# Kernel optimization log

Measured on AMD Instinct MI355X. Metric: run time of the kernel, lower is better.

The kernel has to match this reference:

```python
import jax, jax.numpy as jnp
import numpy as np

BLOCK = 16  # NVFP4 block size (per-block FP8 scale over 16 FP4 values)
FP4_GRID = jnp.array([0.0, 0.5, 1.0, 1.5, 2.0, 3.0, 4.0, 6.0], dtype=jnp.float32)
FP4_MIDS = jnp.array([0.25, 0.75, 1.25, 1.75, 2.5, 3.5, 5.0], dtype=jnp.float32)


def _quantize_fp4(v):
    # round-to-nearest onto the signed E2M1 grid {0,.5,1,1.5,2,3,4,6}
    a = jnp.clip(jnp.abs(v), 0.0, 6.0)
    idx = jnp.searchsorted(FP4_MIDS, a)
    return jnp.sign(v) * FP4_GRID[idx]


def _block_quantize(x):
    # returns (fp4 values, per-16-block scales) such that x ~= q * scale_blocked
    M, K = x.shape
    B = K // BLOCK
    xb = x.reshape(M, B, BLOCK)
    s = jnp.max(jnp.abs(xb), axis=-1) / 6.0 + 1e-8  # [M, B]
    q = _quantize_fp4(xb / s[:, :, None]).reshape(M, K)
    return q, s


def setup_inputs() -> dict:
    key = jax.random.key(0)
    k1, k2, k3 = jax.random.split(key, 3)
    M, K, N = 8192, 4096, 4096
    bsz, q_len = 4, 2048

    x_raw = jax.random.normal(k1, (M, K), dtype=jnp.float32)
    w_raw = jax.random.normal(k2, (N, K), dtype=jnp.float32) * 0.02

    # global weight scale as in NVFP4_reorder_quantize_w: max(w)/(448*6)
    scale_w_global = jnp.max(w_raw) / (448.0 * 6.0)
    qw, scale_w = _block_quantize(w_raw / scale_w_global)

    # activation global scale (produced upstream by the activation quantizer)
    scale_x_global = jnp.max(x_raw) / (448.0 * 6.0)
    qx, scale_x = _block_quantize(x_raw / scale_x_global)

    bias = jax.random.normal(k3, (N,), dtype=jnp.float32) * 0.01

    return {
        "qx": qx,                      # [M, K] FP4-grid values
        "scale_x": scale_x,            # [M, K//16] block scales
        "scale": scale_x_global,       # scalar global activation scale
        "qw": qw,                      # [N, K] FP4-grid values
        "scale_w": scale_w,            # [N, K//16] block scales
        "scale_w_global": scale_w_global,
        "bias": bias,                  # [N]
        "bsz": bsz,
        "q_len": q_len,
    }


def reference(qx, scale_x, scale, qw, scale_w, scale_w_global, bias, bsz, q_len):
    # Dequant-scaled GEMM: y = (qx .* sx)(qw .* sw)^T * (scale * scale_w_global) + bias
    M, K = qx.shape
    N = qw.shape[0]
    B = K // BLOCK
    xd = (qx.reshape(M, B, BLOCK) * scale_x[:, :, None]).reshape(M, K)
    wd = (qw.reshape(N, B, BLOCK) * scale_w[:, :, None]).reshape(N, K)
    y = jnp.einsum("mk,nk->mn", xd, wd) * (scale * scale_w_global)
    y = y + bias
    return y.reshape(bsz, q_len, -1)
```

## Files before the change

### kernel.cpp

```cpp
#include <hip/hip_runtime.h>
#include <cstdint>

#define K_DIM 4096
#define ROWB 13
#define NT   (K_DIM / 64)

typedef __bf16 bf16x8 __attribute__((ext_vector_type(8)));
typedef float f32x4 __attribute__((ext_vector_type(4)));

__device__ inline unsigned short f2bf(float f) {
    union { float f; unsigned int u; } v; v.f = f;
    unsigned int u = v.u;
    return (unsigned short)((u + 0x7FFFu + ((u >> 16) & 1u)) >> 16);
}

__device__ __forceinline__ void gload16(const void* g, void* l) {
    __builtin_amdgcn_global_load_lds(
        (const __attribute__((address_space(1))) unsigned int*)g,
        (__attribute__((address_space(3))) unsigned int*)l,
        16, 0, 0);
}

__global__ __launch_bounds__(256) void dequant2_kernel(
        const float* __restrict__ qx, const float* __restrict__ sx,
        unsigned short* __restrict__ xd, long t8x,
        const float* __restrict__ qw, const float* __restrict__ sw,
        unsigned short* __restrict__ wd, long t8w) {
    long i = (long)blockIdx.x * blockDim.x + threadIdx.x;
    if (i >= t8x + t8w) return;
    const float* q; const float* s; unsigned short* o;
    if (i < t8x) { q = qx; s = sx; o = xd; }
    else         { q = qw; s = sw; o = wd; i -= t8x; }
    long e = i * 8;
    float sc = s[e >> 4];
    float4 v0 = *(const float4*)(q + e);
    float4 v1 = *(const float4*)(q + e + 4);
    union { unsigned short h[8]; uint4 u; } ov;
    ov.h[0] = f2bf(v0.x * sc); ov.h[1] = f2bf(v0.y * sc);
    ov.h[2] = f2bf(v0.z * sc); ov.h[3] = f2bf(v0.w * sc);
    ov.h[4] = f2bf(v1.x * sc); ov.h[5] = f2bf(v1.y * sc);
    ov.h[6] = f2bf(v1.z * sc); ov.h[7] = f2bf(v1.w * sc);
    *(uint4*)(o + e) = ov.u;
}


__global__ __launch_bounds__(512, 2) void gemm256_kernel(
        const unsigned short* __restrict__ A,
        const unsigned short* __restrict__ B,
        const float* __restrict__ sg1, const float* __restrict__ sg2,
        const float* __restrict__ bias,
        float* __restrict__ out, int M, int N) {
    __shared__ __align__(16) char lds[131072];

    const int tid  = threadIdx.x;
    const int lane = tid & 63;
    const int wid  = tid >> 6;
    const int wm   = wid >> 2;
    const int wn   = wid & 3;
    const int l15  = lane & 15;
    const int cb4  = lane >> 4;
    const int rx   = l15 & 7;
    const int xk0  = (cb4 ^ rx) << 4;
    const int xk1  = ((4 + cb4) ^ rx) << 4;

    const int nbn = N >> 8;
    const int nwg = (M >> 8) * nbn;
    const int cpx = nwg >> 3;
    const int bid = blockIdx.x;
    const int swz = (bid & 7) * cpx + (bid >> 3);
    const int tile_m = (swz / nbn) << 8;
    const int tile_n = (swz % nbn) << 8;

    const int scb = ((lane & 7) ^ ((lane >> 3) & 7)) << 4;
    const char* gA1 = (const char*)A +
        ((size_t)(tile_m + wm * 128 + wn * 16 + (lane >> 3)) << ROWB) + scb;
    const char* gA2 = gA1 + ((size_t)64 << ROWB);
    const char* gBs = (const char*)B +
        ((size_t)(tile_n + wn * 64 + wm * 32 + (lane >> 3)) << ROWB) + scb;
    const int dA1 = (wm * 128 + wn * 16) * 128;
    const int dA2 = dA1 + 8192;
    const int dB  = 32768 + (wn * 64 + wm * 32) * 128;

    const int aB = (wm * 128 + l15) * 128;
    const int bB = 32768 + (wn * 64 + l15) * 128;

    f32x4 acc[8][4];
#pragma unroll
    for (int mb = 0; mb < 8; ++mb)
#pragma unroll
        for (int nb = 0; nb < 4; ++nb) acc[mb][nb] = (f32x4){0.f, 0.f, 0.f, 0.f};

    gload16(gA1, lds + dA1);
    gload16(gA1 + ((size_t)8 << ROWB), lds + dA1 + 1024);
    gload16(gBs, lds + dB);
    gload16(gBs + ((size_t)8 << ROWB), lds + dB + 1024);
    gload16(gBs + ((size_t)16 << ROWB), lds + dB + 2048);
    gload16(gBs + ((size_t)24 << ROWB), lds + dB + 3072);
    gload16(gA2, lds + dA2);
    gload16(gA2 + ((size_t)8 << ROWB), lds + dA2 + 1024);
    asm volatile("s_waitcnt vmcnt(0)" ::: "memory");
    __builtin_amdgcn_s_barrier();

#define TILE_BODY(T, CB, SB) do {                                            \
    const int ts_ = ((T) + 1 < NT) ? (T) + 1 : NT - 1;                       \
    const size_t tso = (size_t)ts_ * 128;                                    \
    bf16x8 af[8], af2[8], bf[4], bf2[4];                                     \
      \
    _Pragma("unroll")                                                        \
    for (int mb = 0; mb < 4; ++mb) {                                         \
        af[mb * 2 + 0] = *(const bf16x8*)(lds + (CB) + aB + mb * 2048 + xk0);\
        af[mb * 2 + 1] = *(const bf16x8*)(lds + (CB) + aB + mb * 2048 + xk1);\
    }                                                                        \
    _Pragma("unroll")                                                        \
    for (int nb = 0; nb < 2; ++nb) {                                         \
        bf[nb * 2 + 0] = *(const bf16x8*)(lds + (CB) + bB + nb * 2048 + xk0);\
        bf[nb * 2 + 1] = *(const bf16x8*)(lds + (CB) + bB + nb * 2048 + xk1);\
    }                                                                        \
    gload16(gA1 + tso, lds + (SB) + dA1);                                    \
    gload16(gA1 + tso + ((size_t)8 << ROWB), lds + (SB) + dA1 + 1024);       \
    __builtin_amdgcn_s_barrier();                                            \
    asm volatile("s_waitcnt lgkmcnt(0)" ::: "memory");                       \
    __builtin_amdgcn_s_setprio(1);                                           \
    _Pragma("unroll")                                                        \
    for (int mb = 0; mb < 4; ++mb)                                           \
        _Pragma("unroll")                                                    \
        for (int nb = 0; nb < 2; ++nb)                                       \
            _Pragma("unroll")                                                \
            for (int ks = 0; ks < 2; ++ks)                                   \
                acc[mb][nb] = __builtin_amdgcn_mfma_f32_16x16x32_bf16(       \
                    af[mb * 2 + ks], bf[nb * 2 + ks], acc[mb][nb], 0, 0, 0); \
    __builtin_amdgcn_s_setprio(0);                                           \
    __builtin_amdgcn_s_barrier();                                            \
        \
    _Pragma("unroll")                                                        \
    for (int nb = 0; nb < 2; ++nb) {                                         \
        bf2[nb * 2 + 0] =                                                    \
            *(const bf16x8*)(lds + (CB) + bB + 4096 + nb * 2048 + xk0);      \
        bf2[nb * 2 + 1] =                                                    \
            *(const bf16x8*)(lds + (CB) + bB + 4096 + nb * 2048 + xk1);      \
    }                                                                        \
    gload16(gBs + tso, lds + (SB) + dB);                                     \
    gload16(gBs + tso + ((size_t)8 << ROWB), lds + (SB) + dB + 1024);        \
    __builtin_amdgcn_s_barrier();                                            \
    asm volatile("s_waitcnt lgkmcnt(0)" ::: "memory");                       \
    __builtin_amdgcn_s_setprio(1);                                           \
    _Pragma("unroll")                                                        \
    for (int mb = 0; mb < 4; ++mb)                                           \
        _Pragma("unroll")                                                    \
        for (int nb = 0; nb < 2; ++nb)                                       \
            _Pragma("unroll")                                                \
            for (int ks = 0; ks < 2; ++ks)                                   \
                acc[mb][2 + nb] = __builtin_amdgcn_mfma_f32_16x16x32_bf16(   \
                    af[mb * 2 + ks], bf2[nb * 2 + ks], acc[mb][2 + nb],      \
                    0, 0, 0);                                                \
    __builtin_amdgcn_s_setprio(0);                                           \
    asm volatile("s_waitcnt vmcnt(4)" ::: "memory");                         \
    __builtin_amdgcn_s_barrier();                                            \
        \
    _Pragma("unroll")                                                        \
    for (int mb = 0; mb < 4; ++mb) {                                         \
        af2[mb * 2 + 0] =                                                    \
            *(const bf16x8*)(lds + (CB) + aB + 8192 + mb * 2048 + xk0);      \
        af2[mb * 2 + 1] =                                                    \
            *(const bf16x8*)(lds + (CB) + aB + 8192 + mb * 2048 + xk1);      \
    }                                                                        \
    gload16(gBs + tso + ((size_t)16 << ROWB), lds + (SB) + dB + 2048);       \
    gload16(gBs + tso + ((size_t)24 << ROWB), lds + (SB) + dB + 3072);       \
    __builtin_amdgcn_s_barrier();                                            \
    asm volatile("s_waitcnt lgkmcnt(0)" ::: "memory");                       \
    __builtin_amdgcn_s_setprio(1);                                           \
    _Pragma("unroll")                                                        \
    for (int mb = 0; mb < 4; ++mb)                                           \
        _Pragma("unroll")                                                    \
        for (int nb = 0; nb < 2; ++nb)                                       \
            _Pragma("unroll")                                                \
            for (int ks = 0; ks < 2; ++ks)                                   \
                acc[4 + mb][2 + nb] = __builtin_amdgcn_mfma_f32_16x16x32_bf16(\
                    af2[mb * 2 + ks], bf2[nb * 2 + ks], acc[4 + mb][2 + nb], \
                    0, 0, 0);                                                \
    __builtin_amdgcn_s_setprio(0);                                           \
    __builtin_amdgcn_s_barrier();                                            \
      \
    gload16(gA2 + tso, lds + (SB) + dA2);                                    \
    gload16(gA2 + tso + ((size_t)8 << ROWB), lds + (SB) + dA2 + 1024);       \
    __builtin_amdgcn_s_setprio(1);                                           \
    _Pragma("unroll")                                                        \
    for (int mb = 0; mb < 4; ++mb)                                           \
        _Pragma("unroll")                                                    \
        for (int nb = 0; nb < 2; ++nb)                                       \
            _Pragma("unroll")                                                \
            for (int ks = 0; ks < 2; ++ks)                                   \
                acc[4 + mb][nb] = __builtin_amdgcn_mfma_f32_16x16x32_bf16(   \
                    af2[mb * 2 + ks], bf[nb * 2 + ks], acc[4 + mb][nb],      \
                    0, 0, 0);                                                \
    __builtin_amdgcn_s_setprio(0);                                           \
    asm volatile("s_waitcnt vmcnt(2)" ::: "memory");                         \
    __builtin_amdgcn_s_barrier();                                            \
} while (0)

    for (int t = 0; t < NT; t += 2) {
        TILE_BODY(t,     0,     65536);
        TILE_BODY(t + 1, 65536, 0);
    }
#undef TILE_BODY

    const float gs = sg1[0] * sg2[0];
    const int row0 = tile_m + wm * 128 + (cb4 << 2);
    const int col0 = tile_n + wn * 64 + l15;
    float bv[4];
#pragma unroll
    for (int nb = 0; nb < 4; ++nb) bv[nb] = bias[col0 + nb * 16];
#pragma unroll
    for (int mb = 0; mb < 8; ++mb)
#pragma unroll
        for (int nb = 0; nb < 4; ++nb) {
            const int col = col0 + nb * 16;
#pragma unroll
            for (int j = 0; j < 4; ++j)
                out[(size_t)(row0 + mb * 16 + j) * N + col] =
                    acc[mb][nb][j] * gs + bv[nb];
        }
}

__global__ __launch_bounds__(256) void gemm_fused_kernel(
        const float* __restrict__ qx, const float* __restrict__ sx,
        const float* __restrict__ qw, const float* __restrict__ sw,
        const float* __restrict__ sg1, const float* __restrict__ sg2,
        const float* __restrict__ bias,
        float* __restrict__ out, int M, int N) {
    __shared__ __align__(16) unsigned short As[128 * 32];
    __shared__ __align__(16) unsigned short Bs[128 * 32];
    const int tid  = threadIdx.x;
    const int lane = tid & 63;
    const int wid  = tid >> 6;
    const int tile_n = blockIdx.x * 128;
    const int tile_m = blockIdx.y * 128;
    const int wm = wid >> 1, wn = wid & 1;
    f32x4 acc[16];
#pragma unroll
    for (int i = 0; i < 16; ++i) acc[i] = (f32x4){0.f, 0.f, 0.f, 0.f};
    const int l15 = lane & 15;
    const int lk  = (lane >> 4) * 8;
    for (int kt = 0; kt < K_DIM / 32; ++kt) {
#pragma unroll
        for (int cc = 0; cc < 2; ++cc) {
            const int c   = tid + cc * 256;
            const int row = c >> 2;
            const int col = (c & 3) * 8;
            const int gk  = kt * 32 + col;
            {
                const float* qp = qx + (long)(tile_m + row) * K_DIM + gk;
                float s = sx[(long)(tile_m + row) * (K_DIM / 16) + (gk >> 4)];
                float4 a0 = *(const float4*)qp;
                float4 a1 = *(const float4*)(qp + 4);
                union { unsigned short h[8]; uint4 u; } o;
                o.h[0] = f2bf(a0.x * s); o.h[1] = f2bf(a0.y * s);
                o.h[2] = f2bf(a0.z * s); o.h[3] = f2bf(a0.w * s);
                o.h[4] = f2bf(a1.x * s); o.h[5] = f2bf(a1.y * s);
                o.h[6] = f2bf(a1.z * s); o.h[7] = f2bf(a1.w * s);
                *(uint4*)&As[row * 32 + col] = o.u;
            }
            {
                const float* qp = qw + (long)(tile_n + row) * K_DIM + gk;
                float s = sw[(long)(tile_n + row) * (K_DIM / 16) + (gk >> 4)];
                float4 a0 = *(const float4*)qp;
                float4 a1 = *(const float4*)(qp + 4);
                union { unsigned short h[8]; uint4 u; } o;
                o.h[0] = f2bf(a0.x * s); o.h[1] = f2bf(a0.y * s);
                o.h[2] = f2bf(a0.z * s); o.h[3] = f2bf(a0.w * s);
                o.h[4] = f2bf(a1.x * s); o.h[5] = f2bf(a1.y * s);
                o.h[6] = f2bf(a1.z * s); o.h[7] = f2bf(a1.w * s);
                *(uint4*)&Bs[row * 32 + col] = o.u;
            }
        }
        __syncthreads();
        const unsigned short* pa = As + (wm * 64 + l15) * 32 + lk;
        const unsigned short* pb = Bs + (wn * 64 + l15) * 32 + lk;
        bf16x8 a[4], b[4];
#pragma unroll
        for (int i = 0; i < 4; ++i) {
            a[i] = *(const bf16x8*)(pa + i * 16 * 32);
            b[i] = *(const bf16x8*)(pb + i * 16 * 32);
        }
#pragma unroll
        for (int mi = 0; mi < 4; ++mi)
#pragma unroll
            for (int ni = 0; ni < 4; ++ni)
                acc[mi * 4 + ni] = __builtin_amdgcn_mfma_f32_16x16x32_bf16(
                    a[mi], b[ni], acc[mi * 4 + ni], 0, 0, 0);
        __syncthreads();
    }
    const float gs = sg1[0] * sg2[0];
    const int row0 = tile_m + wm * 64 + (lane >> 4) * 4;
    const int col0 = tile_n + wn * 64 + l15;
#pragma unroll
    for (int mi = 0; mi < 4; ++mi)
#pragma unroll
        for (int ni = 0; ni < 4; ++ni) {
            const int col = col0 + ni * 16;
            const float bv = bias[col];
#pragma unroll
            for (int j = 0; j < 4; ++j)
                out[(long)(row0 + mi * 16 + j) * N + col] =
                    acc[mi * 4 + ni][j] * gs + bv;
        }
}

extern "C" void kernel_launch(void* const* d_in, const int* in_sizes, int n_in,
                              void* d_out, int out_size, void* d_ws, size_t ws_size,
                              hipStream_t stream) {
    const float* qx   = (const float*)d_in[0];
    const float* sx   = (const float*)d_in[1];
    const float* sc   = (const float*)d_in[2];
    const float* qw   = (const float*)d_in[3];
    const float* sw   = (const float*)d_in[4];
    const float* swg  = (const float*)d_in[5];
    const float* bias = (const float*)d_in[6];
    float* out = (float*)d_out;

    const int M = in_sizes[0] / K_DIM;
    const int N = in_sizes[3] / K_DIM;

    const size_t needA = (size_t)M * K_DIM * sizeof(unsigned short);
    const size_t needB = (size_t)N * K_DIM * sizeof(unsigned short);

    if (ws_size >= needA + needB) {
        unsigned short* xd = (unsigned short*)d_ws;
        unsigned short* wd = (unsigned short*)((char*)d_ws + needA);
        long t8x = (long)M * K_DIM / 8;
        long t8w = (long)N * K_DIM / 8;
        long tot = t8x + t8w;
        dequant2_kernel<<<(int)((tot + 255) / 256), 256, 0, stream>>>(
            qx, sx, xd, t8x, qw, sw, wd, t8w);
        const int nwg = (M / 256) * (N / 256);
        gemm256_kernel<<<nwg, 512, 0, stream>>>(xd, wd, sc, swg, bias, out, M, N);
    } else {
        dim3 grid(N / 128, M / 128);
        gemm_fused_kernel<<<grid, 256, 0, stream>>>(
            qx, sx, qw, sw, sc, swg, bias, out, M, N);
    }
}
```

Measured before the change: 272.1 us.

## Switch GEMM inner loop from 16x16x32 to 32x32x16 bf16 MFMA tiles

Replaces the 16x16x32 bf16 MFMA micro-tiles with 32x32x16 MFMAs. The LDS fragment read addressing, the XOR swizzle offsets, the accumulator layout (f32x16) and the epilogue store mapping change to match. The larger MFMA shape reuses each loaded fragment across more output elements, which cuts LDS reads and MFMA issue count per flop. In exchange, bank-conflict behaviour changes under the new swizzle, and the epilogue writes follow a different row/column pattern.

```diff
diff --git a/kernel.cpp b/kernel.cpp
--- a/kernel.cpp
+++ b/kernel.cpp
@@ -6,7 +6,8 @@
 #define NT   (K_DIM / 64)
 
 typedef __bf16 bf16x8 __attribute__((ext_vector_type(8)));
-typedef float f32x4 __attribute__((ext_vector_type(4)));
+typedef float f32x4  __attribute__((ext_vector_type(4)));
+typedef float f32x16 __attribute__((ext_vector_type(16)));
 
 __device__ inline unsigned short f2bf(float f) {
     union { float f; unsigned int u; } v; v.f = f;
@@ -57,11 +58,13 @@
     const int wid  = tid >> 6;
     const int wm   = wid >> 2;
     const int wn   = wid & 3;
-    const int l15  = lane & 15;
-    const int cb4  = lane >> 4;
-    const int rx   = l15 & 7;
-    const int xk0  = (cb4 ^ rx) << 4;
-    const int xk1  = ((4 + cb4) ^ rx) << 4;
+    const int l31  = lane & 31;
+    const int lhi  = lane >> 5;
+    const int rl7  = lane & 7;
+    const int xs0 = ((0 + lhi) ^ rl7) << 4;
+    const int xs1 = ((2 + lhi) ^ rl7) << 4;
+    const int xs2 = ((4 + lhi) ^ rl7) << 4;
+    const int xs3 = ((6 + lhi) ^ rl7) << 4;
 
     const int nbn = N >> 8;
     const int nwg = (M >> 8) * nbn;
@@ -81,14 +84,16 @@
     const int dA2 = dA1 + 8192;
     const int dB  = 32768 + (wn * 64 + wm * 32) * 128;
 
-    const int aB = (wm * 128 + l15) * 128;
-    const int bB = 32768 + (wn * 64 + l15) * 128;
-
-    f32x4 acc[8][4];
-#pragma unroll
-    for (int mb = 0; mb < 8; ++mb)
-#pragma unroll
-        for (int nb = 0; nb < 4; ++nb) acc[mb][nb] = (f32x4){0.f, 0.f, 0.f, 0.f};
+    const int aB = (wm * 128 + l31) * 128;
+    const int bB = 32768 + (wn * 64 + l31) * 128;
+
+    f32x16 acc[4][2];
+#pragma unroll
+    for (int mb = 0; mb < 4; ++mb)
+#pragma unroll
+        for (int nb = 0; nb < 2; ++nb)
+#pragma unroll
+            for (int j = 0; j < 16; ++j) acc[mb][nb][j] = 0.f;
 
     gload16(gA1, lds + dA1);
     gload16(gA1 + ((size_t)8 << ROWB), lds + dA1 + 1024);
@@ -101,68 +106,62 @@
     asm volatile("s_waitcnt vmcnt(0)" ::: "memory");
     __builtin_amdgcn_s_barrier();
 
+#define RD(P) *(const bf16x8*)(P)
 #define TILE_BODY(T, CB, SB) do {                                            \
     const int ts_ = ((T) + 1 < NT) ? (T) + 1 : NT - 1;                       \
     const size_t tso = (size_t)ts_ * 128;                                    \
-    bf16x8 af[8], af2[8], bf[4], bf2[4];                                     \
-      \
-    _Pragma("unroll")                                                        \
-    for (int mb = 0; mb < 4; ++mb) {                                         \
-        af[mb * 2 + 0] = *(const bf16x8*)(lds + (CB) + aB + mb * 2048 + xk0);\
-        af[mb * 2 + 1] = *(const bf16x8*)(lds + (CB) + aB + mb * 2048 + xk1);\
+    bf16x8 af[2][4], af2[2][4], bf[4], bf2[4];                               \
+        \
+    _Pragma("unroll")                                                        \
+    for (int mb = 0; mb < 2; ++mb) {                                         \
+        af[mb][0] = RD(lds + (CB) + aB + mb * 4096 + xs0);                   \
+        af[mb][1] = RD(lds + (CB) + aB + mb * 4096 + xs1);                   \
+        af[mb][2] = RD(lds + (CB) + aB + mb * 4096 + xs2);                   \
+        af[mb][3] = RD(lds + (CB) + aB + mb * 4096 + xs3);                   \
     }                                                                        \
-    _Pragma("unroll")                                                        \
-    for (int nb = 0; nb < 2; ++nb) {                                         \
-        bf[nb * 2 + 0] = *(const bf16x8*)(lds + (CB) + bB + nb * 2048 + xk0);\
-        bf[nb * 2 + 1] = *(const bf16x8*)(lds + (CB) + bB + nb * 2048 + xk1);\
-    }                                                                        \
+    bf[0] = RD(lds + (CB) + bB + xs0);                                       \
+    bf[1] = RD(lds + (CB) + bB + xs1);                                       \
+    bf[2] = RD(lds + (CB) + bB + xs2);                                       \
+    bf[3] = RD(lds + (CB) + bB + xs3);                                       \
     gload16(gA1 + tso, lds + (SB) + dA1);                                    \
     gload16(gA1 + tso + ((size_t)8 << ROWB), lds + (SB) + dA1 + 1024);       \
     __builtin_amdgcn_s_barrier();                                            \
     asm volatile("s_waitcnt lgkmcnt(0)" ::: "memory");                       \
     __builtin_amdgcn_s_setprio(1);                                           \
     _Pragma("unroll")                                                        \
-    for (int mb = 0; mb < 4; ++mb)                                           \
+    for (int s = 0; s < 4; ++s)                                              \
         _Pragma("unroll")                                                    \
-        for (int nb = 0; nb < 2; ++nb)                                       \
-            _Pragma("unroll")                                                \
-            for (int ks = 0; ks < 2; ++ks)                                   \
-                acc[mb][nb] = __builtin_amdgcn_mfma_f32_16x16x32_bf16(       \
-                    af[mb * 2 + ks], bf[nb * 2 + ks], acc[mb][nb], 0, 0, 0); \
+        for (int mb = 0; mb < 2; ++mb)                                       \
+            acc[mb][0] = __builtin_amdgcn_mfma_f32_32x32x16_bf16(            \
+                af[mb][s], bf[s], acc[mb][0], 0, 0, 0);                      \
     __builtin_amdgcn_s_setprio(0);                                           \
     __builtin_amdgcn_s_barrier();                                            \
-        \
-    _Pragma("unroll")                                                        \
-    for (int nb = 0; nb < 2; ++nb) {                                         \
-        bf2[nb * 2 + 0] =                                                    \
-            *(const bf16x8*)(lds + (CB) + bB + 4096 + nb * 2048 + xk0);      \
-        bf2[nb * 2 + 1] =                                                    \
-            *(const bf16x8*)(lds + (CB) + bB + 4096 + nb * 2048 + xk1);      \
-    }                                                                        \
+                \
+    bf2[0] = RD(lds + (CB) + bB + 4096 + xs0);                               \
+    bf2[1] = RD(lds + (CB) + bB + 4096 + xs1);                               \
+    bf2[2] = RD(lds + (CB) + bB + 4096 + xs2);                               \
+    bf2[3] = RD(lds + (CB) + bB + 4096 + xs3);                               \
     gload16(gBs + tso, lds + (SB) + dB);                                     \
     gload16(gBs + tso + ((size_t)8 << ROWB), lds + (SB) + dB + 1024);        \
     __builtin_amdgcn_s_barrier();                                            \
     asm volatile("s_waitcnt lgkmcnt(0)" ::: "memory");                       \
     __builtin_amdgcn_s_setprio(1);                                           \
     _Pragma("unroll")                                                        \
-    for (int mb = 0; mb < 4; ++mb)                                           \
+    for (int s = 0; s < 4; ++s)                                              \
         _Pragma("unroll")                                                    \
-        for (int nb = 0; nb < 2; ++nb)                                       \
-            _Pragma("unroll")                                                \
-            for (int ks = 0; ks < 2; ++ks)                                   \
-                acc[mb][2 + nb] = __builtin_amdgcn_mfma_f32_16x16x32_bf16(   \
-                    af[mb * 2 + ks], bf2[nb * 2 + ks], acc[mb][2 + nb],      \
-                    0, 0, 0);                                                \
+        for (int mb = 0; mb < 2; ++mb)                                       \
+            acc[mb][1] = __builtin_amdgcn_mfma_f32_32x32x16_bf16(            \
+                af[mb][s], bf2[s], acc[mb][1], 0, 0, 0);                     \
     __builtin_amdgcn_s_setprio(0);                                           \
     asm volatile("s_waitcnt vmcnt(4)" ::: "memory");                         \
     __builtin_amdgcn_s_barrier();                                            \
-        \
-    _Pragma("unroll")                                                        \
-    for (int mb = 0; mb < 4; ++mb) {                                         \
-        af2[mb * 2 + 0] =                                                    \
-            *(const bf16x8*)(lds + (CB) + aB + 8192 + mb * 2048 + xk0);      \
-        af2[mb * 2 + 1] =                                                    \
-            *(const bf16x8*)(lds + (CB) + aB + 8192 + mb * 2048 + xk1);      \
+                \
+    _Pragma("unroll")                                                        \
+    for (int mb = 0; mb < 2; ++mb) {                                         \
+        af2[mb][0] = RD(lds + (CB) + aB + 8192 + mb * 4096 + xs0);           \
+        af2[mb][1] = RD(lds + (CB) + aB + 8192 + mb * 4096 + xs1);           \
+        af2[mb][2] = RD(lds + (CB) + aB + 8192 + mb * 4096 + xs2);           \
+        af2[mb][3] = RD(lds + (CB) + aB + 8192 + mb * 4096 + xs3);           \
     }                                                                        \
     gload16(gBs + tso + ((size_t)16 << ROWB), lds + (SB) + dB + 2048);       \
     gload16(gBs + tso + ((size_t)24 << ROWB), lds + (SB) + dB + 3072);       \
@@ -170,29 +169,23 @@
     asm volatile("s_waitcnt lgkmcnt(0)" ::: "memory");                       \
     __builtin_amdgcn_s_setprio(1);                                           \
     _Pragma("unroll")                                                        \
-    for (int mb = 0; mb < 4; ++mb)                                           \
+    for (int s = 0; s < 4; ++s)                                              \
         _Pragma("unroll")                                                    \
-        for (int nb = 0; nb < 2; ++nb)                                       \
-            _Pragma("unroll")                                                \
-            for (int ks = 0; ks < 2; ++ks)                                   \
-                acc[4 + mb][2 + nb] = __builtin_amdgcn_mfma_f32_16x16x32_bf16(\
-                    af2[mb * 2 + ks], bf2[nb * 2 + ks], acc[4 + mb][2 + nb], \
-                    0, 0, 0);                                                \
+        for (int mb = 0; mb < 2; ++mb)                                       \
+            acc[2 + mb][1] = __builtin_amdgcn_mfma_f32_32x32x16_bf16(        \
+                af2[mb][s], bf2[s], acc[2 + mb][1], 0, 0, 0);                \
     __builtin_amdgcn_s_setprio(0);                                           \
     __builtin_amdgcn_s_barrier();                                            \
-      \
+                \
     gload16(gA2 + tso, lds + (SB) + dA2);                                    \
     gload16(gA2 + tso + ((size_t)8 << ROWB), lds + (SB) + dA2 + 1024);       \
     __builtin_amdgcn_s_setprio(1);                                           \
     _Pragma("unroll")                                                        \
-    for (int mb = 0; mb < 4; ++mb)                                           \
+    for (int s = 0; s < 4; ++s)                                              \
         _Pragma("unroll")                                                    \
-        for (int nb = 0; nb < 2; ++nb)                                       \
-            _Pragma("unroll")                                                \
-            for (int ks = 0; ks < 2; ++ks)                                   \
-                acc[4 + mb][nb] = __builtin_amdgcn_mfma_f32_16x16x32_bf16(   \
-                    af2[mb * 2 + ks], bf[nb * 2 + ks], acc[4 + mb][nb],      \
-                    0, 0, 0);                                                \
+        for (int mb = 0; mb < 2; ++mb)                                       \
+            acc[2 + mb][0] = __builtin_amdgcn_mfma_f32_32x32x16_bf16(        \
+                af2[mb][s], bf[s], acc[2 + mb][0], 0, 0, 0);                 \
     __builtin_amdgcn_s_setprio(0);                                           \
     asm volatile("s_waitcnt vmcnt(2)" ::: "memory");                         \
     __builtin_amdgcn_s_barrier();                                            \
@@ -203,22 +196,27 @@
         TILE_BODY(t + 1, 65536, 0);
     }
 #undef TILE_BODY
+#undef RD
 
     const float gs = sg1[0] * sg2[0];
-    const int row0 = tile_m + wm * 128 + (cb4 << 2);
-    const int col0 = tile_n + wn * 64 + l15;
-    float bv[4];
-#pragma unroll
-    for (int nb = 0; nb < 4; ++nb) bv[nb] = bias[col0 + nb * 16];
-#pragma unroll
-    for (int mb = 0; mb < 8; ++mb)
-#pragma unroll
-        for (int nb = 0; nb < 4; ++nb) {
-            const int col = col0 + nb * 16;
-#pragma unroll
-            for (int j = 0; j < 4; ++j)
-                out[(size_t)(row0 + mb * 16 + j) * N + col] =
-                    acc[mb][nb][j] * gs + bv[nb];
+    const int row0 = tile_m + wm * 128 + 4 * lhi;
+    const int col0 = tile_n + wn * 64 + l31;
+    float bv[2];
+#pragma unroll
+    for (int nb = 0; nb < 2; ++nb) bv[nb] = bias[col0 + nb * 32];
+#pragma unroll
+    for (int mb = 0; mb < 4; ++mb)
+#pragma unroll
+        for (int nb = 0; nb < 2; ++nb) {
+            const int col = col0 + nb * 32;
+#pragma unroll
+            for (int g = 0; g < 4; ++g)
+#pragma unroll
+                for (int r = 0; r < 4; ++r) {
+                    const int row = row0 + mb * 32 + 8 * g + r;
+                    out[(size_t)row * N + col] =
+                        acc[mb][nb][g * 4 + r] * gs + bv[nb];
+                }
         }
 }
 
```

After: 309.3 us. 1.14x slower.

## Merge four MFMA phases per K-tile into two with fewer barriers

Applied to the files above, without the earlier changes.

The per-tile main loop is restructured from four compute phases into two. Each phase now loads both halves of one operand from LDS and issues the matching global-to-LDS prefetches together, then runs a merged MFMA cluster that interleaves accumulators. This halves the number of workgroup barriers and waitcnt stalls per K-tile and gives each MFMA burst more independent work. In exchange, each burst needs more live fragment registers, and the prefetch issue order changes, so the vmcnt thresholds depend on the new load ordering.

```diff
diff --git a/kernel.cpp b/kernel.cpp
--- a/kernel.cpp
+++ b/kernel.cpp
@@ -90,10 +90,10 @@
 #pragma unroll
         for (int nb = 0; nb < 4; ++nb) acc[mb][nb] = (f32x4){0.f, 0.f, 0.f, 0.f};
 
+    gload16(gBs, lds + dB);
+    gload16(gBs + ((size_t)8 << ROWB), lds + dB + 1024);
     gload16(gA1, lds + dA1);
     gload16(gA1 + ((size_t)8 << ROWB), lds + dA1 + 1024);
-    gload16(gBs, lds + dB);
-    gload16(gBs + ((size_t)8 << ROWB), lds + dB + 1024);
     gload16(gBs + ((size_t)16 << ROWB), lds + dB + 2048);
     gload16(gBs + ((size_t)24 << ROWB), lds + dB + 3072);
     gload16(gA2, lds + dA2);
@@ -115,25 +115,6 @@
     for (int nb = 0; nb < 2; ++nb) {                                         \
         bf[nb * 2 + 0] = *(const bf16x8*)(lds + (CB) + bB + nb * 2048 + xk0);\
         bf[nb * 2 + 1] = *(const bf16x8*)(lds + (CB) + bB + nb * 2048 + xk1);\
-    }                                                                        \
-    gload16(gA1 + tso, lds + (SB) + dA1);                                    \
-    gload16(gA1 + tso + ((size_t)8 << ROWB), lds + (SB) + dA1 + 1024);       \
-    __builtin_amdgcn_s_barrier();                                            \
-    asm volatile("s_waitcnt lgkmcnt(0)" ::: "memory");                       \
-    __builtin_amdgcn_s_setprio(1);                                           \
-    _Pragma("unroll")                                                        \
-    for (int mb = 0; mb < 4; ++mb)                                           \
-        _Pragma("unroll")                                                    \
-        for (int nb = 0; nb < 2; ++nb)                                       \
-            _Pragma("unroll")                                                \
-            for (int ks = 0; ks < 2; ++ks)                                   \
-                acc[mb][nb] = __builtin_amdgcn_mfma_f32_16x16x32_bf16(       \
-                    af[mb * 2 + ks], bf[nb * 2 + ks], acc[mb][nb], 0, 0, 0); \
-    __builtin_amdgcn_s_setprio(0);                                           \
-    __builtin_amdgcn_s_barrier();                                            \
-        \
-    _Pragma("unroll")                                                        \
-    for (int nb = 0; nb < 2; ++nb) {                                         \
         bf2[nb * 2 + 0] =                                                    \
             *(const bf16x8*)(lds + (CB) + bB + 4096 + nb * 2048 + xk0);      \
         bf2[nb * 2 + 1] =                                                    \
@@ -141,22 +122,29 @@
     }                                                                        \
     gload16(gBs + tso, lds + (SB) + dB);                                     \
     gload16(gBs + tso + ((size_t)8 << ROWB), lds + (SB) + dB + 1024);        \
+    gload16(gA1 + tso, lds + (SB) + dA1);                                    \
+    gload16(gA1 + tso + ((size_t)8 << ROWB), lds + (SB) + dA1 + 1024);       \
+    asm volatile("s_waitcnt lgkmcnt(8)" ::: "memory");                       \
     __builtin_amdgcn_s_barrier();                                            \
     asm volatile("s_waitcnt lgkmcnt(0)" ::: "memory");                       \
     __builtin_amdgcn_s_setprio(1);                                           \
     _Pragma("unroll")                                                        \
     for (int mb = 0; mb < 4; ++mb)                                           \
         _Pragma("unroll")                                                    \
-        for (int nb = 0; nb < 2; ++nb)                                       \
+        for (int ks = 0; ks < 2; ++ks) {                                     \
             _Pragma("unroll")                                                \
-            for (int ks = 0; ks < 2; ++ks)                                   \
+            for (int nb = 0; nb < 2; ++nb) {                                 \
+                acc[mb][nb] = __builtin_amdgcn_mfma_f32_16x16x32_bf16(       \
+                    af[mb * 2 + ks], bf[nb * 2 + ks], acc[mb][nb], 0, 0, 0); \
                 acc[mb][2 + nb] = __builtin_amdgcn_mfma_f32_16x16x32_bf16(   \
                     af[mb * 2 + ks], bf2[nb * 2 + ks], acc[mb][2 + nb],      \
                     0, 0, 0);                                                \
+            }                                                                \
+        }                                                                    \
     __builtin_amdgcn_s_setprio(0);                                           \
-    asm volatile("s_waitcnt vmcnt(4)" ::: "memory");                         \
+    asm volatile("s_waitcnt vmcnt(4)" ::: "memory");     \
     __builtin_amdgcn_s_barrier();                                            \
-        \
+           \
     _Pragma("unroll")                                                        \
     for (int mb = 0; mb < 4; ++mb) {                                         \
         af2[mb * 2 + 0] =                                                    \
@@ -166,35 +154,27 @@
     }                                                                        \
     gload16(gBs + tso + ((size_t)16 << ROWB), lds + (SB) + dB + 2048);       \
     gload16(gBs + tso + ((size_t)24 << ROWB), lds + (SB) + dB + 3072);       \
+    gload16(gA2 + tso, lds + (SB) + dA2);                                    \
+    gload16(gA2 + tso + ((size_t)8 << ROWB), lds + (SB) + dA2 + 1024);       \
     __builtin_amdgcn_s_barrier();                                            \
     asm volatile("s_waitcnt lgkmcnt(0)" ::: "memory");                       \
     __builtin_amdgcn_s_setprio(1);                                           \
     _Pragma("unroll")                                                        \
     for (int mb = 0; mb < 4; ++mb)                                           \
         _Pragma("unroll")                                                    \
-        for (int nb = 0; nb < 2; ++nb)                                       \
+        for (int ks = 0; ks < 2; ++ks) {                                     \
             _Pragma("unroll")                                                \
-            for (int ks = 0; ks < 2; ++ks)                                   \
+            for (int nb = 0; nb < 2; ++nb) {                                 \
                 acc[4 + mb][2 + nb] = __builtin_amdgcn_mfma_f32_16x16x32_bf16(\
                     af2[mb * 2 + ks], bf2[nb * 2 + ks], acc[4 + mb][2 + nb], \
                     0, 0, 0);                                                \
-    __builtin_amdgcn_s_setprio(0);                                           \
-    __builtin_amdgcn_s_barrier();                                            \
-      \
-    gload16(gA2 + tso, lds + (SB) + dA2);                                    \
-    gload16(gA2 + tso + ((size_t)8 << ROWB), lds + (SB) + dA2 + 1024);       \
-    __builtin_amdgcn_s_setprio(1);                                           \
-    _Pragma("unroll")                                                        \
-    for (int mb = 0; mb < 4; ++mb)                                           \
-        _Pragma("unroll")                                                    \
-        for (int nb = 0; nb < 2; ++nb)                                       \
-            _Pragma("unroll")                                                \
-            for (int ks = 0; ks < 2; ++ks)                                   \
                 acc[4 + mb][nb] = __builtin_amdgcn_mfma_f32_16x16x32_bf16(   \
                     af2[mb * 2 + ks], bf[nb * 2 + ks], acc[4 + mb][nb],      \
                     0, 0, 0);                                                \
+            }                                                                \
+        }                                                                    \
     __builtin_amdgcn_s_setprio(0);                                           \
-    asm volatile("s_waitcnt vmcnt(2)" ::: "memory");                         \
+    asm volatile("s_waitcnt vmcnt(2)" ::: "memory");  \
     __builtin_amdgcn_s_barrier();                                            \
 } while (0)
 
```

Result: slower. 281.2 us (+3.3%).
